# Optimization experiments

Measured on AMD Instinct MI355X. Metric: run time of the kernel, lower is better.

## Reference

```python
import jax, jax.numpy as jnp
import numpy as np

D_MODEL = 2048
NUM_HEADS = 32
NUM_KV_HEADS = 8
HEAD_DIM = D_MODEL // NUM_HEADS  # 64
GROUP = NUM_HEADS // NUM_KV_HEADS  # 4


def setup_inputs() -> dict:
    key = jax.random.key(0)
    ks = jax.random.split(key, 9)
    s = 1.0 / np.sqrt(D_MODEL)
    kv_dim = NUM_KV_HEADS * HEAD_DIM
    return {
        "x": jax.random.normal(ks[0], (2, 2048, D_MODEL), dtype=jnp.float32),
        "Wq": jax.random.normal(ks[1], (D_MODEL, D_MODEL), dtype=jnp.float32) * s,
        "bq": jnp.zeros((D_MODEL,), dtype=jnp.float32),
        "Wk": jax.random.normal(ks[2], (D_MODEL, kv_dim), dtype=jnp.float32) * s,
        "bk": jnp.zeros((kv_dim,), dtype=jnp.float32),
        "Wv": jax.random.normal(ks[3], (D_MODEL, kv_dim), dtype=jnp.float32) * s,
        "bv": jnp.zeros((kv_dim,), dtype=jnp.float32),
        "Wo": jax.random.normal(ks[4], (D_MODEL, D_MODEL), dtype=jnp.float32) * s,
        "bo": jnp.zeros((D_MODEL,), dtype=jnp.float32),
    }


def reference(x, Wq, bq, Wk, bk, Wv, bv, Wo, bo):
    B, S, _ = x.shape
    # projections
    q = (x @ Wq + bq).reshape(B, S, NUM_HEADS, HEAD_DIM).transpose(0, 2, 1, 3)      # [B,H,S,Dh]
    k = (x @ Wk + bk).reshape(B, S, NUM_KV_HEADS, HEAD_DIM).transpose(0, 2, 1, 3)   # [B,Hkv,S,Dh]
    v = (x @ Wv + bv).reshape(B, S, NUM_KV_HEADS, HEAD_DIM).transpose(0, 2, 1, 3)
    # expand KV heads to match query heads (repeat_interleave along head dim)
    k = jnp.repeat(k, GROUP, axis=1)  # [B,H,S,Dh]
    v = jnp.repeat(v, GROUP, axis=1)
    scale = 1.0 / np.sqrt(HEAD_DIM).astype(np.float32)
    scores = jnp.einsum('bhqd,bhkd->bhqk', q, k) * scale  # [B,H,S,S]
    attn = jax.nn.softmax(scores, axis=-1)
    out = jnp.einsum('bhqk,bhkd->bhqd', attn, v)          # [B,H,S,Dh]
    out = out.transpose(0, 2, 1, 3).reshape(B, S, NUM_HEADS * HEAD_DIM)
    return out @ Wo + bo
```

## Files before the change

### kernel.cpp

```cpp
#include <hip/hip_runtime.h>
#include <stdint.h>

typedef unsigned short u16;
typedef unsigned int u32;
typedef short bf16x8 __attribute__((ext_vector_type(8)));
typedef float f32x4 __attribute__((ext_vector_type(4)));
typedef u32 u32x2 __attribute__((ext_vector_type(2)));

#define GLOAD_LDS16(gptr, lptr)                                                \
  __builtin_amdgcn_global_load_lds(                                            \
      (__attribute__((address_space(1))) void*)(gptr),                         \
      (__attribute__((address_space(3))) void*)(lptr), 16, 0, 0)

#if __has_builtin(__builtin_amdgcn_exp2f)
#define EXP2F(x) __builtin_amdgcn_exp2f(x)
#else
#define EXP2F(x) exp2f(x)
#endif

__device__ __forceinline__ u16 f2bf(float f) {
  union { float f; uint32_t u; } v; v.f = f;
  return (u16)((v.u + 0x7fffu + ((v.u >> 16) & 1u)) >> 16);
}
__device__ __forceinline__ float bf2f(u16 h) {
  union { uint32_t u; float f; } v; v.u = ((uint32_t)h) << 16;
  return v.f;
}
__device__ __forceinline__ u32 cvt_pk_bf16(float lo, float hi) {
  u32 r;
  asm("v_cvt_pk_bf16_f32 %0, %1, %2" : "=v"(r) : "v"(lo), "v"(hi));
  return r;
}

__global__ void k_conv_bf16(const float* __restrict__ src, u16* __restrict__ dst, int n8) {
  int i = blockIdx.x * blockDim.x + threadIdx.x;
  if (i >= n8) return;
  const float4* s = (const float4*)src + (size_t)i * 2;
  float4 a = s[0], b = s[1];
  uint4 o;
  o.x = (uint32_t)f2bf(a.x) | ((uint32_t)f2bf(a.y) << 16);
  o.y = (uint32_t)f2bf(a.z) | ((uint32_t)f2bf(a.w) << 16);
  o.z = (uint32_t)f2bf(b.x) | ((uint32_t)f2bf(b.y) << 16);
  o.w = (uint32_t)f2bf(b.z) | ((uint32_t)f2bf(b.w) << 16);
  ((uint4*)dst)[i] = o;
}

__global__ void k_transpose_bf16(const float* __restrict__ src, u16* __restrict__ dst,
                                 int R, int C) {
  __shared__ float tile[32][33];
  int cb = blockIdx.x * 32, rb = blockIdx.y * 32;
  int tx = threadIdx.x, ty = threadIdx.y;
#pragma unroll
  for (int j = 0; j < 4; ++j)
    tile[ty + j * 8][tx] = src[(size_t)(rb + ty + j * 8) * C + cb + tx];
  __syncthreads();
#pragma unroll
  for (int j = 0; j < 4; ++j)
    dst[(size_t)(cb + ty + j * 8) * R + rb + tx] = f2bf(tile[tx][ty + j * 8]);
}

__global__ void k_transpose_v(const u16* __restrict__ cqkv, u16* __restrict__ vt) {
  __shared__ u16 tile[32][34];
  int st = blockIdx.x, dt = blockIdx.y, bk = blockIdx.z;
  int b = bk >> 3, kvh = bk & 7;
  int tx = threadIdx.x, ty = threadIdx.y;
  const u16* src = cqkv + (size_t)(b * 2048 + st * 32) * 3072 + 2560 + kvh * 64 + dt * 32;
#pragma unroll
  for (int j = 0; j < 4; ++j)
    tile[ty + j * 8][tx] = src[(size_t)(ty + j * 8) * 3072 + tx];
  __syncthreads();
  u16* dst = vt + ((size_t)(bk * 64 + dt * 32)) * 2048 + st * 32;
#pragma unroll
  for (int j = 0; j < 4; ++j)
    dst[(size_t)(ty + j * 8) * 2048 + tx] = tile[tx][ty + j * 8];
}

template <bool BF16OUT>
__global__ __launch_bounds__(256) void k_gemm_bt(
    const u16* __restrict__ A, const u16* __restrict__ Bt,
    const float* __restrict__ bias, void* __restrict__ Cptr,
    int M, int N, int K, int gx, int nwg) {
  __shared__ u16 As[2][128 * 32];
  __shared__ u16 Bs[2][128 * 32];
  const int t = threadIdx.x;
  const int lane = t & 63;
  const int w = t >> 6, wr = w >> 1, wc = w & 1;
  const int bid = blockIdx.x;
  const int cpx = nwg >> 3;
  const int swz = (bid & 7) * cpx + (bid >> 3);
  const int brow = (swz / gx) * 128, bcol = (swz % gx) * 128;
  const int g = lane >> 4, q = lane & 15;

  f32x4 acc[4][4] = {};
  const int srow = t >> 2;
  const int sj = t & 3;
  const int nkt = K >> 5;

  auto stage = [&](int bb, int kt_) {
#pragma unroll
    for (int i = 0; i < 2; ++i) {
      int row = srow + i * 64;
      int jsrc = sj ^ ((row >> 1) & 3);
      const u16* ga = A + (size_t)(brow + row) * K + kt_ * 32 + jsrc * 8;
      const u16* gb = Bt + (size_t)(bcol + row) * K + kt_ * 32 + jsrc * 8;
      GLOAD_LDS16(ga, (char*)(&As[bb][0]) + i * 4096 + t * 16);
      GLOAD_LDS16(gb, (char*)(&Bs[bb][0]) + i * 4096 + t * 16);
    }
  };

  stage(0, 0);
  __syncthreads();
  int cur = 0;

  for (int kt = 0; kt < nkt; ++kt) {
    if (kt < nkt - 1) stage(cur ^ 1, kt + 1);
    const u16* Ac = As[cur];
    const u16* Bc = Bs[cur];
    bf16x8 a[4], b[4];
#pragma unroll
    for (int mt = 0; mt < 4; ++mt) {
      int row = wr * 64 + mt * 16 + q;
      int pos = g ^ ((row >> 1) & 3);
      a[mt] = *(const bf16x8*)(Ac + row * 32 + pos * 8);
    }
#pragma unroll
    for (int nt = 0; nt < 4; ++nt) {
      int row = wc * 64 + nt * 16 + q;
      int pos = g ^ ((row >> 1) & 3);
      b[nt] = *(const bf16x8*)(Bc + row * 32 + pos * 8);
    }
    __builtin_amdgcn_s_setprio(1);
#pragma unroll
    for (int mt = 0; mt < 4; ++mt)
#pragma unroll
      for (int nt = 0; nt < 4; ++nt)
        acc[mt][nt] = __builtin_amdgcn_mfma_f32_16x16x32_bf16(a[mt], b[nt], acc[mt][nt], 0, 0, 0);
    __builtin_amdgcn_s_setprio(0);
    __syncthreads();
    cur ^= 1;
  }
#pragma unroll
  for (int nt = 0; nt < 4; ++nt) {
    int col = bcol + wc * 64 + nt * 16 + q;
    float bv_ = bias[col];
#pragma unroll
    for (int mt = 0; mt < 4; ++mt) {
#pragma unroll
      for (int r = 0; r < 4; ++r) {
        int row = brow + wr * 64 + mt * 16 + g * 4 + r;
        float val = acc[mt][nt][r] + bv_;
        if (BF16OUT)
          ((u16*)Cptr)[(size_t)row * N + col] = f2bf(val);
        else
          ((float*)Cptr)[(size_t)row * N + col] = val;
      }
    }
  }
}

#define LOG2E 1.44269504088896340736f
__global__ __launch_bounds__(256) void k_attn(const u16* __restrict__ qkv,
                                              const u16* __restrict__ vt,
                                              u16* __restrict__ out) {
  const int qt = blockIdx.x, h = blockIdx.y, b = blockIdx.z;
  const int kvh = h >> 2;
  const int t = threadIdx.x, lane = t & 63, w = t >> 6;
  const int g = lane >> 4, q16 = lane & 15;
  const int LDQ = 3072;

  __shared__ u16 Ksh[2][64 * 64];
  __shared__ u16 Vsh[2][64 * 64];
  __shared__ u16 Psh[4][16 * 72] __attribute__((aligned(16)));

  bf16x8 qf[4][2];
#pragma unroll
  for (int s = 0; s < 4; ++s) {
    const size_t qrow = (size_t)(b * 2048 + qt * 256 + s * 64 + w * 16 + q16);
#pragma unroll
    for (int c = 0; c < 2; ++c) {
      bf16x8 tmp = *(const bf16x8*)(qkv + qrow * LDQ + h * 64 + c * 32 + g * 8);
#pragma unroll
      for (int i = 0; i < 8; ++i)
        tmp[i] = (short)f2bf(bf2f((u16)tmp[i]) * 0.125f);
      qf[s][c] = tmp;
    }
  }

  f32x4 acc[4][4] = {};
  float m_run[4], l_run[4];
#pragma unroll
  for (int s = 0; s < 4; ++s) { m_run[s] = -__builtin_inff(); l_run[s] = 0.f; }

  const int kbase = b * 2048;
  const int koff = 2048 + kvh * 64;
  const u16* vtb = vt + (size_t)((b * 8 + kvh) * 64) * 2048;
  const int srow = t >> 3;
  const int sj = t & 7;
  const int cx = sj ^ (srow & 7);

  const u16* gk = qkv + (size_t)(kbase + srow) * LDQ + koff + cx * 8;
  const u16* gv = vtb + (size_t)srow * 2048 + cx * 8;

  auto stage = [&](int bb) {
    GLOAD_LDS16(gk,               (char*)(&Ksh[bb][0]) + t * 16);
    GLOAD_LDS16(gk + 32 * LDQ,    (char*)(&Ksh[bb][0]) + 4096 + t * 16);
    GLOAD_LDS16(gv,               (char*)(&Vsh[bb][0]) + t * 16);
    GLOAD_LDS16(gv + 32 * 2048,   (char*)(&Vsh[bb][0]) + 4096 + t * 16);
  };

  stage(0);
  gk += 64 * LDQ; gv += 64;
  __syncthreads();
  int cur = 0;

  for (int kt = 0; kt < 32; ++kt) {
    if (kt < 31) { stage(cur ^ 1); gk += 64 * LDQ; gv += 64; }
    const u16* Kc = Ksh[cur];
    const u16* Vc = Vsh[cur];

#pragma unroll
    for (int p2 = 0; p2 < 2; ++p2) {
      const int s0 = p2 * 2, s1 = p2 * 2 + 1;
      f32x4 sc[2][4] = {};
      __builtin_amdgcn_s_setprio(1);
#pragma unroll
      for (int c = 0; c < 2; ++c) {
#pragma unroll
        for (int nt = 0; nt < 4; ++nt) {
          int row = nt * 16 + q16;
          bf16x8 kf = *(const bf16x8*)(Kc + row * 64 + (((c * 4 + g) ^ (row & 7)) << 3));
          sc[0][nt] = __builtin_amdgcn_mfma_f32_16x16x32_bf16(kf, qf[s0][c], sc[0][nt], 0, 0, 0);
          sc[1][nt] = __builtin_amdgcn_mfma_f32_16x16x32_bf16(kf, qf[s1][c], sc[1][nt], 0, 0, 0);
        }
      }
      __builtin_amdgcn_s_setprio(0);

      bf16x8 pf[2][2];
#pragma unroll
      for (int i2 = 0; i2 < 2; ++i2) {
        const int s = p2 * 2 + i2;
        float mt_ = sc[i2][0][0];
#pragma unroll
        for (int nt = 0; nt < 4; ++nt)
#pragma unroll
          for (int r = 0; r < 4; ++r)
            mt_ = fmaxf(mt_, sc[i2][nt][r]);
        mt_ = fmaxf(mt_, __shfl_xor(mt_, 16, 64));
        mt_ = fmaxf(mt_, __shfl_xor(mt_, 32, 64));
        if (__any(mt_ > m_run[s])) {
          float mn = fmaxf(m_run[s], mt_);
          float alpha = EXP2F((m_run[s] - mn) * LOG2E);
          m_run[s] = mn;
          l_run[s] *= alpha;
#pragma unroll
          for (int r = 0; r < 4; ++r) {
            float ar = __shfl(alpha, g * 4 + r, 64);
#pragma unroll
            for (int dt = 0; dt < 4; ++dt) acc[s][dt][r] *= ar;
          }
        }
        float mL = m_run[s] * LOG2E;
        float lt = 0.f;
#pragma unroll
        for (int nt = 0; nt < 4; ++nt)
#pragma unroll
          for (int r = 0; r < 4; ++r) {
            float p_ = EXP2F(fmaf(sc[i2][nt][r], LOG2E, -mL));
            sc[i2][nt][r] = p_;
            lt += p_;
          }
        lt += __shfl_xor(lt, 16, 64);
        lt += __shfl_xor(lt, 32, 64);
        l_run[s] += lt;
        u16* prow = &Psh[w][q16 * 72];
#pragma unroll
        for (int nt = 0; nt < 4; ++nt) {
          u32x2 pk;
          pk.x = cvt_pk_bf16(sc[i2][nt][0], sc[i2][nt][1]);
          pk.y = cvt_pk_bf16(sc[i2][nt][2], sc[i2][nt][3]);
          *(u32x2*)(prow + nt * 16 + g * 4) = pk;
        }
        pf[i2][0] = *(const bf16x8*)(&Psh[w][q16 * 72 + g * 8]);
        pf[i2][1] = *(const bf16x8*)(&Psh[w][q16 * 72 + 32 + g * 8]);
      }

      __builtin_amdgcn_s_setprio(1);
#pragma unroll
      for (int c = 0; c < 2; ++c) {
        int kc = c * 4 + g;
#pragma unroll
        for (int dt = 0; dt < 4; ++dt) {
          int d = dt * 16 + q16;
          bf16x8 vf = *(const bf16x8*)(Vc + d * 64 + ((kc ^ (d & 7)) << 3));
          acc[s0][dt] = __builtin_amdgcn_mfma_f32_16x16x32_bf16(pf[0][c], vf, acc[s0][dt], 0, 0, 0);
          acc[s1][dt] = __builtin_amdgcn_mfma_f32_16x16x32_bf16(pf[1][c], vf, acc[s1][dt], 0, 0, 0);
        }
      }
      __builtin_amdgcn_s_setprio(0);
    }

    __syncthreads();
    cur ^= 1;
  }

#pragma unroll
  for (int s = 0; s < 4; ++s)
#pragma unroll
    for (int r = 0; r < 4; ++r) {
      float linv = 1.0f / __shfl(l_run[s], g * 4 + r, 64);
      size_t orow = (size_t)(b * 2048 + qt * 256 + s * 64 + w * 16 + g * 4 + r);
#pragma unroll
      for (int dt = 0; dt < 4; ++dt)
        out[orow * 2048 + h * 64 + dt * 16 + q16] = f2bf(acc[s][dt][r] * linv);
    }
}

extern "C" void kernel_launch(void* const* d_in, const int* in_sizes, int n_in,
                              void* d_out, int out_size, void* d_ws, size_t ws_size,
                              hipStream_t stream) {
  const float* x  = (const float*)d_in[0];
  const float* Wq = (const float*)d_in[1];
  const float* bq = (const float*)d_in[2];
  const float* Wk = (const float*)d_in[3];
  const float* bk = (const float*)d_in[4];
  const float* Wv = (const float*)d_in[5];
  const float* bv = (const float*)d_in[6];
  const float* Wo = (const float*)d_in[7];
  const float* bo = (const float*)d_in[8];
  float* out = (float*)d_out;

  char* ws = (char*)d_ws;
  u16*   xb    = (u16*)(ws + 0);
  u16*   wqkvT = (u16*)(ws + 16777216);
  u16*   woT   = (u16*)(ws + 29360128);
  float* bqkv  = (float*)(ws + 37748736);
  u16*   cqkv  = (u16*)(ws + 37761024);
  u16*   aout  = (u16*)(ws + 62926848);
  u16*   vtb   = xb;
  (void)ws_size; (void)in_sizes; (void)n_in; (void)out_size;

  hipMemcpyAsync(bqkv, bq, 2048 * sizeof(float), hipMemcpyDeviceToDevice, stream);
  hipMemcpyAsync(bqkv + 2048, bk, 512 * sizeof(float), hipMemcpyDeviceToDevice, stream);
  hipMemcpyAsync(bqkv + 2560, bv, 512 * sizeof(float), hipMemcpyDeviceToDevice, stream);

  k_conv_bf16<<<4096, 256, 0, stream>>>(x, xb, 1048576);
  dim3 tb(32, 8);
  k_transpose_bf16<<<dim3(64, 64), tb, 0, stream>>>(Wq, wqkvT, 2048, 2048);
  k_transpose_bf16<<<dim3(16, 64), tb, 0, stream>>>(Wk, wqkvT + 2048 * 2048, 2048, 512);
  k_transpose_bf16<<<dim3(16, 64), tb, 0, stream>>>(Wv, wqkvT + 2560 * 2048, 2048, 512);
  k_transpose_bf16<<<dim3(64, 64), tb, 0, stream>>>(Wo, woT, 2048, 2048);

  k_gemm_bt<true><<<768, 256, 0, stream>>>(xb, wqkvT, bqkv, cqkv, 4096, 3072, 2048, 24, 768);
  k_transpose_v<<<dim3(64, 2, 16), tb, 0, stream>>>(cqkv, vtb);
  k_attn<<<dim3(8, 32, 2), 256, 0, stream>>>(cqkv, vtb, aout);
  k_gemm_bt<false><<<512, 256, 0, stream>>>(aout, woT, bo, out, 4096, 2048, 2048, 16, 512);
}
```

Measured before the change: 372.5 us.

## Triple-buffer LDS staging with partial vmcnt waits in GEMM and attention

Both the projection GEMM and the attention kernel move from double to triple buffering of their LDS tiles, so loads run two tiles ahead. The full __syncthreads drain is replaced by s_waitcnt vmcnt(4) plus a raw s_barrier, which keeps the newest stage's loads in flight across the barrier. This is meant to hide global-to-LDS latency better, at the cost of more LDS per block (possibly lower occupancy) and a dependence on exact per-thread load counts for correctness.

Result: no change. 369.0 us (-0.9%).

```diff
diff --git a/kernel.cpp b/kernel.cpp
--- a/kernel.cpp
+++ b/kernel.cpp
@@ -11,6 +11,9 @@
   __builtin_amdgcn_global_load_lds(                                            \
       (__attribute__((address_space(1))) void*)(gptr),                         \
       (__attribute__((address_space(3))) void*)(lptr), 16, 0, 0)
+
+#define WAITV4() asm volatile("s_waitcnt vmcnt(4)" ::: "memory")
+#define WAITV0() asm volatile("s_waitcnt vmcnt(0)" ::: "memory")
 
 #if __has_builtin(__builtin_amdgcn_exp2f)
 #define EXP2F(x) __builtin_amdgcn_exp2f(x)
@@ -80,8 +83,8 @@
     const u16* __restrict__ A, const u16* __restrict__ Bt,
     const float* __restrict__ bias, void* __restrict__ Cptr,
     int M, int N, int K, int gx, int nwg) {
-  __shared__ u16 As[2][128 * 32];
-  __shared__ u16 Bs[2][128 * 32];
+  __shared__ u16 As[3][128 * 32];
+  __shared__ u16 Bs[3][128 * 32];
   const int t = threadIdx.x;
   const int lane = t & 63;
   const int w = t >> 6, wr = w >> 1, wc = w & 1;
@@ -94,26 +97,28 @@
   f32x4 acc[4][4] = {};
   const int srow = t >> 2;
   const int sj = t & 3;
+  const int jx = sj ^ ((srow >> 1) & 3);
   const int nkt = K >> 5;
 
-  auto stage = [&](int bb, int kt_) {
-#pragma unroll
-    for (int i = 0; i < 2; ++i) {
-      int row = srow + i * 64;
-      int jsrc = sj ^ ((row >> 1) & 3);
-      const u16* ga = A + (size_t)(brow + row) * K + kt_ * 32 + jsrc * 8;
-      const u16* gb = Bt + (size_t)(bcol + row) * K + kt_ * 32 + jsrc * 8;
-      GLOAD_LDS16(ga, (char*)(&As[bb][0]) + i * 4096 + t * 16);
-      GLOAD_LDS16(gb, (char*)(&Bs[bb][0]) + i * 4096 + t * 16);
-    }
+  const u16* gA = A + (size_t)(brow + srow) * K + jx * 8;
+  const u16* gB = Bt + (size_t)(bcol + srow) * K + jx * 8;
+
+  auto stage = [&](int bb) {
+    GLOAD_LDS16(gA,                     (char*)(&As[bb][0]) + t * 16);
+    GLOAD_LDS16(gA + (size_t)64 * K,    (char*)(&As[bb][0]) + 4096 + t * 16);
+    GLOAD_LDS16(gB,                     (char*)(&Bs[bb][0]) + t * 16);
+    GLOAD_LDS16(gB + (size_t)64 * K,    (char*)(&Bs[bb][0]) + 4096 + t * 16);
+    gA += 32; gB += 32;
   };
 
-  stage(0, 0);
-  __syncthreads();
+  stage(0);
+  stage(1);
+  WAITV4();
+  __builtin_amdgcn_s_barrier();
+  __builtin_amdgcn_sched_barrier(0);
+
   int cur = 0;
-
   for (int kt = 0; kt < nkt; ++kt) {
-    if (kt < nkt - 1) stage(cur ^ 1, kt + 1);
     const u16* Ac = As[cur];
     const u16* Bc = Bs[cur];
     bf16x8 a[4], b[4];
@@ -129,6 +134,10 @@
       int pos = g ^ ((row >> 1) & 3);
       b[nt] = *(const bf16x8*)(Bc + row * 32 + pos * 8);
     }
+    if (kt + 2 < nkt) {
+      int b2 = cur + 2; if (b2 >= 3) b2 -= 3;
+      stage(b2);
+    }
     __builtin_amdgcn_s_setprio(1);
 #pragma unroll
     for (int mt = 0; mt < 4; ++mt)
@@ -136,8 +145,12 @@
       for (int nt = 0; nt < 4; ++nt)
         acc[mt][nt] = __builtin_amdgcn_mfma_f32_16x16x32_bf16(a[mt], b[nt], acc[mt][nt], 0, 0, 0);
     __builtin_amdgcn_s_setprio(0);
-    __syncthreads();
-    cur ^= 1;
+    if (kt + 1 < nkt) {
+      if (kt + 2 < nkt) WAITV4(); else WAITV0();
+      __builtin_amdgcn_s_barrier();
+      __builtin_amdgcn_sched_barrier(0);
+    }
+    ++cur; if (cur >= 3) cur -= 3;
   }
 #pragma unroll
   for (int nt = 0; nt < 4; ++nt) {
@@ -168,8 +181,8 @@
   const int g = lane >> 4, q16 = lane & 15;
   const int LDQ = 3072;
 
-  __shared__ u16 Ksh[2][64 * 64];
-  __shared__ u16 Vsh[2][64 * 64];
+  __shared__ u16 Ksh[3][64 * 64];
+  __shared__ u16 Vsh[3][64 * 64];
   __shared__ u16 Psh[4][16 * 72] __attribute__((aligned(16)));
 
   bf16x8 qf[4][2];
@@ -206,15 +219,21 @@
     GLOAD_LDS16(gk + 32 * LDQ,    (char*)(&Ksh[bb][0]) + 4096 + t * 16);
     GLOAD_LDS16(gv,               (char*)(&Vsh[bb][0]) + t * 16);
     GLOAD_LDS16(gv + 32 * 2048,   (char*)(&Vsh[bb][0]) + 4096 + t * 16);
+    gk += 64 * LDQ; gv += 64;
   };
 
   stage(0);
-  gk += 64 * LDQ; gv += 64;
-  __syncthreads();
+  stage(1);
+  WAITV4();
+  __builtin_amdgcn_s_barrier();
+  __builtin_amdgcn_sched_barrier(0);
+
   int cur = 0;
-
   for (int kt = 0; kt < 32; ++kt) {
-    if (kt < 31) { stage(cur ^ 1); gk += 64 * LDQ; gv += 64; }
+    if (kt + 2 < 32) {
+      int b2 = cur + 2; if (b2 >= 3) b2 -= 3;
+      stage(b2);
+    }
     const u16* Kc = Ksh[cur];
     const u16* Vc = Vsh[cur];
 
@@ -299,8 +318,12 @@
       __builtin_amdgcn_s_setprio(0);
     }
 
-    __syncthreads();
-    cur ^= 1;
+    if (kt + 1 < 32) {
+      if (kt + 2 < 32) WAITV4(); else WAITV0();
+      __builtin_amdgcn_s_barrier();
+      __builtin_amdgcn_sched_barrier(0);
+    }
+    ++cur; if (cur >= 3) cur -= 3;
   }
 
 #pragma unroll
```
